# Performance work log

Hardware: AMD Instinct MI355X
Metric: run time of the kernel (lower is better)

The kernel has to match this reference:

```python
import jax, jax.numpy as jnp
import numpy as np

# Spherical-harmonics constants (from _need_const)
A0 = float(np.pi)
A1 = float(2 * np.pi / np.sqrt(3.0))
A2 = float(2 * np.pi / np.sqrt(8.0))
C0 = float(1 / np.sqrt(4 * np.pi))
C1 = float(np.sqrt(3.0) / np.sqrt(4 * np.pi))
C2 = float(3 * np.sqrt(5.0) / np.sqrt(12 * np.pi))
D0 = float(0.5 / np.sqrt(3.0))
# BlendParams defaults (pytorch3d)
SIGMA = 1e-4
GAMMA_B = 1e-4
BG = (1.0, 1.0, 1.0)
ZNEAR, ZFAR, EPS = 1.0, 100.0, 1e-10


def setup_inputs() -> dict:
    key = jax.random.key(0)
    ks = jax.random.split(key, 9)
    N, H, W, K, V, F = 4, 512, 512, 4, 36000, 70000
    texels = jax.random.uniform(ks[0], (N, H, W, K, 3), dtype=jnp.float32)
    b = jax.random.uniform(ks[1], (N, H, W, K, 3), dtype=jnp.float32) + 1e-3
    bary_coords = b / jnp.sum(b, axis=-1, keepdims=True)
    pix_to_face = jax.random.randint(ks[2], (N, H, W, K), -1, F)  # -1 = empty pixel
    zbuf = jax.random.uniform(ks[3], (N, H, W, K), minval=ZNEAR, maxval=ZFAR, dtype=jnp.float32)
    dists = jax.random.normal(ks[4], (N, H, W, K), dtype=jnp.float32) * 1e-4
    verts = jax.random.normal(ks[5], (V, 3), dtype=jnp.float32)
    faces = jax.random.randint(ks[6], (F, 3), 0, V)
    vn = jax.random.normal(ks[7], (V, 3), dtype=jnp.float32)
    vertex_normals = vn / jnp.linalg.norm(vn, axis=-1, keepdims=True)
    gamma = jax.random.normal(ks[8], (N, 27), dtype=jnp.float32) * 0.1
    return dict(texels=texels, bary_coords=bary_coords, zbuf=zbuf, dists=dists,
                verts=verts, vertex_normals=vertex_normals, gamma=gamma,
                pix_to_face=pix_to_face, faces=faces)


def _interp_face_attrs(pix_to_face, bary, attrs):
    # attrs: (F, 3, D); pix_to_face: (N,H,W,K); bary: (N,H,W,K,3)
    mask = (pix_to_face >= 0)
    idx = jnp.where(mask, pix_to_face, 0)
    g = attrs[idx]  # (N,H,W,K,3,D) gather
    out = jnp.einsum('nhwkv,nhwkvd->nhwkd', bary, g)
    return out * mask[..., None].astype(out.dtype)


def reference(texels, bary_coords, zbuf, dists, verts, vertex_normals, gamma, pix_to_face, faces):
    # flip x,y of vertex normals (as in phong_shading)
    vn = vertex_normals * jnp.asarray([-1.0, -1.0, 1.0], vertex_normals.dtype)
    faces_normals = vn[faces]  # (F,3,3)
    pixel_normals = _interp_face_attrs(pix_to_face, bary_coords, faces_normals)  # (N,H,W,K,3)
    # Note: pixel_coords (from verts) is computed in the original but unused since
    # lights/cameras/materials are None -> specular_color = 0.
    g = gamma.reshape(-1, 3, 9)
    g = g.at[:, :, 0].add(0.8)
    g = jnp.transpose(g, (0, 2, 1))  # (N,9,3)
    nx, ny, nz = pixel_normals[..., 0], pixel_normals[..., 1], pixel_normals[..., 2]
    Y = jnp.stack([
        jnp.full_like(nx, A0 * C0),
        -A1 * C1 * ny,
        A1 * C1 * nz,
        -A1 * C1 * nx,
        A2 * C2 * nx * ny,
        -A2 * C2 * ny * nz,
        A2 * C2 * D0 * (3.0 * nz * nz - 1.0),
        -A2 * C2 * nx * nz,
        A2 * C2 * 0.5 * (nx * nx - ny * ny),
    ], axis=-1)  # (N,H,W,K,9)
    lighting = jnp.einsum('nhwki,nij->nhwkj', Y, g)  # (N,H,W,K,3)
    colors = lighting * texels  # specular = 0
    # softmax_rgb_blend (pytorch3d)
    mask = (pix_to_face >= 0).astype(colors.dtype)
    prob = jax.nn.sigmoid(-dists / SIGMA) * mask
    alpha = 1.0 - jnp.prod(1.0 - prob, axis=-1)
    z_inv = (ZFAR - zbuf) / (ZFAR - ZNEAR) * mask
    z_inv_max = jnp.clip(jnp.max(z_inv, axis=-1, keepdims=True), EPS, None)
    w_num = prob * jnp.exp((z_inv - z_inv_max) / GAMMA_B)
    delta = jnp.clip(jnp.exp((EPS - z_inv_max) / GAMMA_B), EPS, None)
    denom = jnp.sum(w_num, axis=-1, keepdims=True) + delta
    weights = w_num / denom  # (N,H,W,K)
    rgb = jnp.einsum('nhwk,nhwkc->nhwc', weights, colors)
    bg = (delta / denom) * jnp.asarray(BG, colors.dtype)  # (N,H,W,3) via broadcast of (N,H,W,1)
    return jnp.concatenate([rgb + bg, alpha[..., None]], axis=-1)  # (N,H,W,4)
```

## Files before the change

kernel.cpp:

```cpp
#include <hip/hip_runtime.h>
#include <math.h>

#define C_A0 3.14159265358979323846f
#define C_A1 3.6275987284684357f
#define C_A2 2.2214414690791831f
#define C_C0 0.28209479177387814f
#define C_C1 0.48860251190291992f
#define C_C2 1.0925484305920792f
#define C_D0 0.28867513459481287f
#define C_SIGMA  1e-4f
#define C_GAMMAB 1e-4f
#define C_ZNEAR  1.0f
#define C_ZFAR   100.0f
#define C_EPS    1e-10f

__global__ __launch_bounds__(256) void build_face_table(
    const int* __restrict__ faces, const float* __restrict__ vn,
    uint4* __restrict__ tbl, int F)
{
    int f = blockIdx.x * 256 + threadIdx.x;
    if (f >= F) return;
    float c[9];
#pragma unroll
    for (int v = 0; v < 3; ++v) {
        int vi = faces[f * 3 + v];
        c[v * 3 + 0] = -vn[vi * 3 + 0];
        c[v * 3 + 1] = -vn[vi * 3 + 1];
        c[v * 3 + 2] =  vn[vi * 3 + 2];
    }
    unsigned qv[9];
#pragma unroll
    for (int i = 0; i < 9; ++i) {
        int q = (int)rintf(c[i] * 8191.0f);
        q = q < -8191 ? -8191 : (q > 8191 ? 8191 : q);
        qv[i] = (unsigned)q & 0x3FFFu;
    }
    unsigned dw[4];
#pragma unroll
    for (int j = 0; j < 4; ++j) {
        unsigned nib = (qv[8] >> (4 * j)) & 0xFu;
        dw[j] = qv[2 * j] | (qv[2 * j + 1] << 14) | (nib << 28);
    }
    tbl[f] = make_uint4(dw[0], dw[1], dw[2], dw[3]);
}

__device__ __forceinline__ float sext14(unsigned dw, int pos)
{
    int v = ((int)(dw << (18 - pos))) >> 18;
    return (float)v * (1.0f / 8191.0f);
}

__device__ __forceinline__ void unpack9(uint4 q, float* __restrict__ c)
{
    unsigned dw[4] = { q.x, q.y, q.z, q.w };
#pragma unroll
    for (int j = 0; j < 4; ++j) {
        c[2 * j]     = sext14(dw[j], 0);
        c[2 * j + 1] = sext14(dw[j], 14);
    }
    unsigned q8 = (dw[0] >> 28) | ((dw[1] >> 28) << 4)
                | ((dw[2] >> 28) << 8) | ((dw[3] >> 28) << 12);
    int v8 = ((int)(q8 << 18)) >> 18;
    c[8] = (float)v8 * (1.0f / 8191.0f);
}

__device__ __forceinline__ float qsum(float v)  { v += __shfl_xor(v, 1); v += __shfl_xor(v, 2); return v; }
__device__ __forceinline__ float qmax4(float v) { v = fmaxf(v, __shfl_xor(v, 1)); v = fmaxf(v, __shfl_xor(v, 2)); return v; }
__device__ __forceinline__ float qprod(float v) { v *= __shfl_xor(v, 1); v *= __shfl_xor(v, 2); return v; }

template <bool USE_TABLE>
__global__ __launch_bounds__(256) void shade_kernel(
    const float* __restrict__ texels,
    const float* __restrict__ bary,
    const float* __restrict__ zbuf,
    const float* __restrict__ dists,
    const float* __restrict__ vn,
    const float* __restrict__ gamma,
    const int*   __restrict__ p2f,
    const int*   __restrict__ faces,
    const uint4* __restrict__ tbl,
    float4* __restrict__ out,
    int nfrag, int hwk)
{
    int f = blockIdx.x * 256 + threadIdx.x;
    if (f >= nfrag) return;
    int n = (blockIdx.x * 256) / hwk;
    const float* __restrict__ g = gamma + n * 27;

    int fc = p2f[f];
    int fi = fc >= 0 ? fc : 0;
    float m = fc >= 0 ? 1.0f : 0.0f;

    float w0 = bary[f * 3 + 0], w1 = bary[f * 3 + 1], w2 = bary[f * 3 + 2];
    float t0 = texels[f * 3 + 0], t1 = texels[f * 3 + 1], t2 = texels[f * 3 + 2];
    float zb = zbuf[f];
    float dd = dists[f];

    float nx, ny, nz;
    if (USE_TABLE) {
        uint4 q = tbl[fi];
        float c[9];
        unpack9(q, c);
        nx = w0 * c[0] + w1 * c[3] + w2 * c[6];
        ny = w0 * c[1] + w1 * c[4] + w2 * c[7];
        nz = w0 * c[2] + w1 * c[5] + w2 * c[8];
    } else {
        nx = 0.0f; ny = 0.0f; nz = 0.0f;
        float wv[3] = { w0, w1, w2 };
#pragma unroll
        for (int v = 0; v < 3; ++v) {
            int vi = faces[fi * 3 + v];
            nx += wv[v] * (-vn[vi * 3 + 0]);
            ny += wv[v] * (-vn[vi * 3 + 1]);
            nz += wv[v] * ( vn[vi * 3 + 2]);
        }
    }
    nx *= m; ny *= m; nz *= m;

    float Yv[9];
    Yv[0] = C_A0 * C_C0;
    Yv[1] = -(C_A1 * C_C1) * ny;
    Yv[2] =  (C_A1 * C_C1) * nz;
    Yv[3] = -(C_A1 * C_C1) * nx;
    Yv[4] =  (C_A2 * C_C2) * nx * ny;
    Yv[5] = -(C_A2 * C_C2) * ny * nz;
    Yv[6] =  (C_A2 * C_C2) * C_D0 * (3.0f * nz * nz - 1.0f);
    Yv[7] = -(C_A2 * C_C2) * nx * nz;
    Yv[8] =  (C_A2 * C_C2) * 0.5f * (nx * nx - ny * ny);

    float tex[3] = { t0, t1, t2 };
    float col[3];
#pragma unroll
    for (int c = 0; c < 3; ++c) {
        float l = Yv[0] * (g[c * 9 + 0] + 0.8f);
#pragma unroll
        for (int i = 1; i < 9; ++i) l += Yv[i] * g[c * 9 + i];
        col[c] = l * tex[c];
    }

    float prob = m * __builtin_amdgcn_rcpf(1.0f + __expf(dd * (1.0f / C_SIGMA)));
    float zinv = (C_ZFAR - zb) * (1.0f / (C_ZFAR - C_ZNEAR)) * m;

    float zmax = fmaxf(qmax4(zinv), C_EPS);
    float wn   = prob * __expf((zinv - zmax) * (1.0f / C_GAMMAB));
    float delta = fmaxf(__expf((C_EPS - zmax) * (1.0f / C_GAMMAB)), C_EPS);

    float denom = qsum(wn) + delta;
    float r  = qsum(wn * col[0]);
    float gc = qsum(wn * col[1]);
    float b  = qsum(wn * col[2]);
    float alpha = 1.0f - qprod(1.0f - prob);

    if ((threadIdx.x & 3) == 0) {
        float inv = __builtin_amdgcn_rcpf(denom);
        out[f >> 2] = make_float4((r + delta) * inv,
                                  (gc + delta) * inv,
                                  (b + delta) * inv,
                                  alpha);
    }
}

extern "C" void kernel_launch(void* const* d_in, const int* in_sizes, int n_in,
                              void* d_out, int out_size, void* d_ws, size_t ws_size,
                              hipStream_t stream) {
    const float* texels = (const float*)d_in[0];
    const float* bary   = (const float*)d_in[1];
    const float* zbuf   = (const float*)d_in[2];
    const float* dists  = (const float*)d_in[3];
    const float* vn     = (const float*)d_in[5];
    const float* gamma  = (const float*)d_in[6];
    const int*   p2f    = (const int*)d_in[7];
    const int*   faces  = (const int*)d_in[8];

    int nfrag = in_sizes[2];
    int N     = in_sizes[6] / 27;
    int hwk   = nfrag / N;
    int F     = in_sizes[8] / 3;

    float4* out = (float4*)d_out;
    size_t tbl_bytes = (size_t)F * sizeof(uint4);

    int shade_blocks = (nfrag + 255) / 256;
    if (ws_size >= tbl_bytes) {
        uint4* tbl = (uint4*)d_ws;
        build_face_table<<<(F + 255) / 256, 256, 0, stream>>>(faces, vn, tbl, F);
        shade_kernel<true><<<shade_blocks, 256, 0, stream>>>(
            texels, bary, zbuf, dists, vn, gamma, p2f, faces, tbl, out, nfrag, hwk);
    } else {
        shade_kernel<false><<<shade_blocks, 256, 0, stream>>>(
            texels, bary, zbuf, dists, vn, gamma, p2f, faces, nullptr, out, nfrag, hwk);
    }
}
```

Baseline: 193.6 us.

## Map one thread per pixel with float4 vector loads instead of per-fragment

Changes the thread mapping from one thread per fragment to one thread per pixel, so each thread handles all K=4 fragments. Inputs are read as float4/int4 vectors (texels and bary as three float4 per pixel), and the cross-lane shuffle reductions become in-register sums. Each thread now issues four independent table gathers, which adds memory-level parallelism. The costs are a quarter as many threads, higher register use and less occupancy to hide gather latency.

```diff
diff --git a/kernel.cpp b/kernel.cpp
--- a/kernel.cpp
+++ b/kernel.cpp
@@ -64,59 +64,10 @@
     c[8] = (float)v8 * (1.0f / 8191.0f);
 }
 
-__device__ __forceinline__ float qsum(float v)  { v += __shfl_xor(v, 1); v += __shfl_xor(v, 2); return v; }
-__device__ __forceinline__ float qmax4(float v) { v = fmaxf(v, __shfl_xor(v, 1)); v = fmaxf(v, __shfl_xor(v, 2)); return v; }
-__device__ __forceinline__ float qprod(float v) { v *= __shfl_xor(v, 1); v *= __shfl_xor(v, 2); return v; }
-
-template <bool USE_TABLE>
-__global__ __launch_bounds__(256) void shade_kernel(
-    const float* __restrict__ texels,
-    const float* __restrict__ bary,
-    const float* __restrict__ zbuf,
-    const float* __restrict__ dists,
-    const float* __restrict__ vn,
-    const float* __restrict__ gamma,
-    const int*   __restrict__ p2f,
-    const int*   __restrict__ faces,
-    const uint4* __restrict__ tbl,
-    float4* __restrict__ out,
-    int nfrag, int hwk)
-{
-    int f = blockIdx.x * 256 + threadIdx.x;
-    if (f >= nfrag) return;
-    int n = (blockIdx.x * 256) / hwk;
-    const float* __restrict__ g = gamma + n * 27;
-
-    int fc = p2f[f];
-    int fi = fc >= 0 ? fc : 0;
-    float m = fc >= 0 ? 1.0f : 0.0f;
-
-    float w0 = bary[f * 3 + 0], w1 = bary[f * 3 + 1], w2 = bary[f * 3 + 2];
-    float t0 = texels[f * 3 + 0], t1 = texels[f * 3 + 1], t2 = texels[f * 3 + 2];
-    float zb = zbuf[f];
-    float dd = dists[f];
-
-    float nx, ny, nz;
-    if (USE_TABLE) {
-        uint4 q = tbl[fi];
-        float c[9];
-        unpack9(q, c);
-        nx = w0 * c[0] + w1 * c[3] + w2 * c[6];
-        ny = w0 * c[1] + w1 * c[4] + w2 * c[7];
-        nz = w0 * c[2] + w1 * c[5] + w2 * c[8];
-    } else {
-        nx = 0.0f; ny = 0.0f; nz = 0.0f;
-        float wv[3] = { w0, w1, w2 };
-#pragma unroll
-        for (int v = 0; v < 3; ++v) {
-            int vi = faces[fi * 3 + v];
-            nx += wv[v] * (-vn[vi * 3 + 0]);
-            ny += wv[v] * (-vn[vi * 3 + 1]);
-            nz += wv[v] * ( vn[vi * 3 + 2]);
-        }
-    }
-    nx *= m; ny *= m; nz *= m;
-
+__device__ __forceinline__ void sh_color(
+    float nx, float ny, float nz, const float* __restrict__ g,
+    float t0, float t1, float t2, float* __restrict__ col)
+{
     float Yv[9];
     Yv[0] = C_A0 * C_C0;
     Yv[1] = -(C_A1 * C_C1) * ny;
@@ -127,9 +78,7 @@
     Yv[6] =  (C_A2 * C_C2) * C_D0 * (3.0f * nz * nz - 1.0f);
     Yv[7] = -(C_A2 * C_C2) * nx * nz;
     Yv[8] =  (C_A2 * C_C2) * 0.5f * (nx * nx - ny * ny);
-
     float tex[3] = { t0, t1, t2 };
-    float col[3];
 #pragma unroll
     for (int c = 0; c < 3; ++c) {
         float l = Yv[0] * (g[c * 9 + 0] + 0.8f);
@@ -137,27 +86,103 @@
         for (int i = 1; i < 9; ++i) l += Yv[i] * g[c * 9 + i];
         col[c] = l * tex[c];
     }
-
-    float prob = m * __builtin_amdgcn_rcpf(1.0f + __expf(dd * (1.0f / C_SIGMA)));
-    float zinv = (C_ZFAR - zb) * (1.0f / (C_ZFAR - C_ZNEAR)) * m;
-
-    float zmax = fmaxf(qmax4(zinv), C_EPS);
-    float wn   = prob * __expf((zinv - zmax) * (1.0f / C_GAMMAB));
+}
+
+template <bool USE_TABLE>
+__global__ __launch_bounds__(256) void shade_pix(
+    const float4* __restrict__ texels,
+    const float4* __restrict__ bary,
+    const float4* __restrict__ zbuf,
+    const float4* __restrict__ dists,
+    const float* __restrict__ vn,
+    const float* __restrict__ gamma,
+    const int4*  __restrict__ p2f,
+    const int*   __restrict__ faces,
+    const uint4* __restrict__ tbl,
+    float4* __restrict__ out,
+    int npix, int hw)
+{
+    int p = blockIdx.x * 256 + threadIdx.x;
+    if (p >= npix) return;
+    int n = (blockIdx.x * 256) / hw;
+    const float* __restrict__ g = gamma + n * 27;
+
+    int4 fq = p2f[p];
+    float4 t0 = texels[3 * p + 0], t1 = texels[3 * p + 1], t2 = texels[3 * p + 2];
+    float4 b0 = bary[3 * p + 0],  b1 = bary[3 * p + 1],  b2 = bary[3 * p + 2];
+    float4 z4 = zbuf[p];
+    float4 d4 = dists[p];
+
+    int   fc[4]  = { fq.x, fq.y, fq.z, fq.w };
+    float tex[12] = { t0.x, t0.y, t0.z, t0.w, t1.x, t1.y, t1.z, t1.w,
+                      t2.x, t2.y, t2.z, t2.w };
+    float w[12]   = { b0.x, b0.y, b0.z, b0.w, b1.x, b1.y, b1.z, b1.w,
+                      b2.x, b2.y, b2.z, b2.w };
+    float zv[4] = { z4.x, z4.y, z4.z, z4.w };
+    float dv[4] = { d4.x, d4.y, d4.z, d4.w };
+
+    float mk[4], col[4][3];
+
+    if (USE_TABLE) {
+        uint4 q[4];
+#pragma unroll
+        for (int k = 0; k < 4; ++k) {
+            int fi = fc[k] >= 0 ? fc[k] : 0;
+            mk[k] = fc[k] >= 0 ? 1.0f : 0.0f;
+            q[k] = tbl[fi];
+        }
+#pragma unroll
+        for (int k = 0; k < 4; ++k) {
+            float c[9];
+            unpack9(q[k], c);
+            float w0 = w[3 * k], w1 = w[3 * k + 1], w2 = w[3 * k + 2];
+            float nx = (w0 * c[0] + w1 * c[3] + w2 * c[6]) * mk[k];
+            float ny = (w0 * c[1] + w1 * c[4] + w2 * c[7]) * mk[k];
+            float nz = (w0 * c[2] + w1 * c[5] + w2 * c[8]) * mk[k];
+            sh_color(nx, ny, nz, g, tex[3 * k], tex[3 * k + 1], tex[3 * k + 2], col[k]);
+        }
+    } else {
+#pragma unroll
+        for (int k = 0; k < 4; ++k) {
+            int fi = fc[k] >= 0 ? fc[k] : 0;
+            mk[k] = fc[k] >= 0 ? 1.0f : 0.0f;
+            float nx = 0.0f, ny = 0.0f, nz = 0.0f;
+#pragma unroll
+            for (int v = 0; v < 3; ++v) {
+                int vi = faces[fi * 3 + v];
+                float wv = w[3 * k + v];
+                nx += wv * (-vn[vi * 3 + 0]);
+                ny += wv * (-vn[vi * 3 + 1]);
+                nz += wv * ( vn[vi * 3 + 2]);
+            }
+            nx *= mk[k]; ny *= mk[k]; nz *= mk[k];
+            sh_color(nx, ny, nz, g, tex[3 * k], tex[3 * k + 1], tex[3 * k + 2], col[k]);
+        }
+    }
+
+    float prob[4], zinv[4];
+#pragma unroll
+    for (int k = 0; k < 4; ++k) {
+        prob[k] = mk[k] * __builtin_amdgcn_rcpf(1.0f + __expf(dv[k] * (1.0f / C_SIGMA)));
+        zinv[k] = (C_ZFAR - zv[k]) * (1.0f / (C_ZFAR - C_ZNEAR)) * mk[k];
+    }
+    float zmax = fmaxf(fmaxf(fmaxf(zinv[0], zinv[1]), fmaxf(zinv[2], zinv[3])), C_EPS);
+
+    float wn[4];
+#pragma unroll
+    for (int k = 0; k < 4; ++k)
+        wn[k] = prob[k] * __expf((zinv[k] - zmax) * (1.0f / C_GAMMAB));
     float delta = fmaxf(__expf((C_EPS - zmax) * (1.0f / C_GAMMAB)), C_EPS);
 
-    float denom = qsum(wn) + delta;
-    float r  = qsum(wn * col[0]);
-    float gc = qsum(wn * col[1]);
-    float b  = qsum(wn * col[2]);
-    float alpha = 1.0f - qprod(1.0f - prob);
-
-    if ((threadIdx.x & 3) == 0) {
-        float inv = __builtin_amdgcn_rcpf(denom);
-        out[f >> 2] = make_float4((r + delta) * inv,
-                                  (gc + delta) * inv,
-                                  (b + delta) * inv,
-                                  alpha);
-    }
+    float denom = (wn[0] + wn[1]) + (wn[2] + wn[3]) + delta;
+    float r  = (wn[0] * col[0][0] + wn[1] * col[1][0]) + (wn[2] * col[2][0] + wn[3] * col[3][0]);
+    float gc = (wn[0] * col[0][1] + wn[1] * col[1][1]) + (wn[2] * col[2][1] + wn[3] * col[3][1]);
+    float b  = (wn[0] * col[0][2] + wn[1] * col[1][2]) + (wn[2] * col[2][2] + wn[3] * col[3][2]);
+    float alpha = 1.0f - ((1.0f - prob[0]) * (1.0f - prob[1]))
+                       * ((1.0f - prob[2]) * (1.0f - prob[3]));
+
+    float inv = __builtin_amdgcn_rcpf(denom);
+    out[p] = make_float4((r + delta) * inv, (gc + delta) * inv, (b + delta) * inv, alpha);
 }
 
 extern "C" void kernel_launch(void* const* d_in, const int* in_sizes, int n_in,
@@ -174,20 +199,25 @@
 
     int nfrag = in_sizes[2];
     int N     = in_sizes[6] / 27;
-    int hwk   = nfrag / N;
     int F     = in_sizes[8] / 3;
+    int npix  = nfrag >> 2;
+    int hw    = npix / N;
 
     float4* out = (float4*)d_out;
     size_t tbl_bytes = (size_t)F * sizeof(uint4);
 
-    int shade_blocks = (nfrag + 255) / 256;
+    int blocks = (npix + 255) / 256;
     if (ws_size >= tbl_bytes) {
         uint4* tbl = (uint4*)d_ws;
         build_face_table<<<(F + 255) / 256, 256, 0, stream>>>(faces, vn, tbl, F);
-        shade_kernel<true><<<shade_blocks, 256, 0, stream>>>(
-            texels, bary, zbuf, dists, vn, gamma, p2f, faces, tbl, out, nfrag, hwk);
+        shade_pix<true><<<blocks, 256, 0, stream>>>(
+            (const float4*)texels, (const float4*)bary, (const float4*)zbuf,
+            (const float4*)dists, vn, gamma, (const int4*)p2f, faces, tbl,
+            out, npix, hw);
     } else {
-        shade_kernel<false><<<shade_blocks, 256, 0, stream>>>(
-            texels, bary, zbuf, dists, vn, gamma, p2f, faces, nullptr, out, nfrag, hwk);
-    }
-}
+        shade_pix<false><<<blocks, 256, 0, stream>>>(
+            (const float4*)texels, (const float4*)bary, (const float4*)zbuf,
+            (const float4*)dists, vn, gamma, (const int4*)p2f, faces, nullptr,
+            out, npix, hw);
+    }
+}
```

New measurement: 196.7 us. Within noise of the previous version (+1.6%).
